# Kernel tuning notes

Hardware: AMD Instinct MI355X
Metric: run time of the kernel (lower is better)

## Reference

```python
import jax, jax.numpy as jnp
import numpy as np

N_HEAD, D_MODEL, D_HEAD = 16, 1024, 64
BSZ, SEQLEN = 2, 2048
ROPE_BASE = 10000.0


def _rope_tables(seqlen, d_head, base=ROPE_BASE):
    # freqs_cis = exp(i * t * theta_j), theta_j = base^(-2j/d_head)
    inv_freq = 1.0 / (base ** (np.arange(0, d_head, 2, dtype=np.float32) / d_head))
    t = np.arange(seqlen, dtype=np.float32)
    ang = np.outer(t, inv_freq)  # [S, d_head//2]
    return jnp.asarray(np.cos(ang)), jnp.asarray(np.sin(ang))


def setup_inputs() -> dict:
    key = jax.random.key(0)
    ks = jax.random.split(key, 5)
    x = jax.random.normal(ks[0], (BSZ, SEQLEN, D_MODEL), dtype=jnp.float32)
    freqs_cos, freqs_sin = _rope_tables(SEQLEN, D_HEAD)
    scale = 0.02
    # weights stored as (in, out) so projection is x @ w
    wq = jax.random.normal(ks[1], (D_MODEL, N_HEAD * D_HEAD), dtype=jnp.float32) * scale
    wk = jax.random.normal(ks[2], (D_MODEL, N_HEAD * D_HEAD), dtype=jnp.float32) * scale
    wv = jax.random.normal(ks[3], (D_MODEL, N_HEAD * D_HEAD), dtype=jnp.float32) * scale
    wo = jax.random.normal(ks[4], (N_HEAD * D_HEAD, D_MODEL), dtype=jnp.float32) * scale
    return {"x": x, "freqs_cos": freqs_cos, "freqs_sin": freqs_sin,
            "wq": wq, "wk": wk, "wv": wv, "wo": wo}


def _apply_rope(t, cos, sin):
    # t: [B, S, H, Dh]; complex pairs are consecutive elements (x0 + i*x1)
    B, S, H, Dh = t.shape
    tf = t.astype(jnp.float32).reshape(B, S, H, Dh // 2, 2)
    t0, t1 = tf[..., 0], tf[..., 1]
    c = cos[None, :, None, :]  # [1, S, 1, Dh//2]
    s = sin[None, :, None, :]
    o0 = t0 * c - t1 * s
    o1 = t0 * s + t1 * c
    return jnp.stack([o0, o1], axis=-1).reshape(B, S, H, Dh).astype(t.dtype)


def reference(x, freqs_cos, freqs_sin, wq, wk, wv, wo):
    B, S, _ = x.shape
    H, Dh = N_HEAD, D_HEAD
    q = jnp.einsum('bsd,de->bse', x, wq).reshape(B, S, H, Dh)
    k = jnp.einsum('bsd,de->bse', x, wk).reshape(B, S, H, Dh)
    v = jnp.einsum('bsd,de->bse', x, wv).reshape(B, S, H, Dh)
    q = _apply_rope(q, freqs_cos, freqs_sin)
    k = _apply_rope(k, freqs_cos, freqs_sin)
    # [B, H, S, Dh]
    q = q.transpose(0, 2, 1, 3)
    k = k.transpose(0, 2, 1, 3)
    v = v.transpose(0, 2, 1, 3)
    scores = jnp.einsum('bhqd,bhkd->bhqk', q, k) / jnp.sqrt(jnp.float32(Dh))
    probs = jax.nn.softmax(scores.astype(jnp.float32), axis=-1).astype(q.dtype)
    out = jnp.einsum('bhqk,bhkd->bhqd', probs, v)  # [B, H, S, Dh]
    out = out.transpose(0, 2, 1, 3).reshape(B, S, H * Dh)
    return jnp.einsum('bse,ed->bsd', out, wo)
```

## Files before the change

kernel.cpp:

```cpp
#include <hip/hip_runtime.h>
#include <math.h>

#define BSZ 2
#define SEQ 2048
#define NH 16
#define DH 64
#define DM 1024
#define HD 1024

typedef _Float16 h16;
typedef _Float16 half8 __attribute__((ext_vector_type(8)));
typedef _Float16 half4 __attribute__((ext_vector_type(4)));
typedef float f32x4 __attribute__((ext_vector_type(4)));
typedef unsigned int u32;
typedef unsigned int u32x2v __attribute__((ext_vector_type(2)));
typedef unsigned int u32x4v __attribute__((ext_vector_type(4)));

__device__ __forceinline__ f32x4 mfma16(half8 a, half8 b, f32x4 c) {
    return __builtin_amdgcn_mfma_f32_16x16x32_f16(a, b, c, 0, 0, 0);
}

__device__ __forceinline__ void async_copy16(h16* lds, const h16* g) {
    __builtin_amdgcn_global_load_lds(
        (const __attribute__((address_space(1))) unsigned int*)g,
        (__attribute__((address_space(3))) unsigned int*)lds, 16, 0, 0);
}

#define SWZ(cb, r) ((((cb) ^ ((r) & 7)) * 8))

#define QSWZ(cb, r) ((((cb) ^ ((r) & 3) ^ (((r) >> 2) & 3)) * 8))

#define OBA(r, c) ((r) * 64 + ((((c) >> 2) ^ ((r) & 15)) << 2))

#define EXP2(x) __builtin_amdgcn_exp2f(x)

__device__ __forceinline__ u32 pack2(float a, float b) {
    auto p = __builtin_amdgcn_cvt_pkrtz(a, b);
    return __builtin_bit_cast(u32, p);
}

__device__ __forceinline__ void pl32swap(u32& a, u32& b) {
#if __has_builtin(__builtin_amdgcn_permlane32_swap)
    u32x2v r = __builtin_amdgcn_permlane32_swap(a, b, false, false);
    a = r.x; b = r.y;
#else
    u32 sa = __builtin_amdgcn_ds_swizzle(a, 0x801F);
    u32 sb = __builtin_amdgcn_ds_swizzle(b, 0x801F);
    bool hi = (threadIdx.x & 32) != 0;
    u32 na = hi ? sb : a;
    u32 nb = hi ? b : sa;
    a = na; b = nb;
#endif
}

__device__ __forceinline__ void pl16swap(u32& a, u32& b) {
#if __has_builtin(__builtin_amdgcn_permlane16_swap)
    u32x2v r = __builtin_amdgcn_permlane16_swap(a, b, false, false);
    a = r.x; b = r.y;
#else
    u32 sa = __builtin_amdgcn_ds_swizzle(a, 0x401F);
    u32 sb = __builtin_amdgcn_ds_swizzle(b, 0x401F);
    bool hi = (threadIdx.x & 16) != 0;
    u32 na = hi ? sb : a;
    u32 nb = hi ? b : sa;
    a = na; b = nb;
#endif
}

__global__ __launch_bounds__(256) void prep_kernel(
    const float* __restrict__ x, const float* __restrict__ wq,
    const float* __restrict__ wk, const float* __restrict__ wv,
    const float* __restrict__ wo,
    h16* __restrict__ x16, h16* __restrict__ wt)
{
    const int z = blockIdx.z;
    const int t = threadIdx.x;
    if (z == 4) {
        int flat = blockIdx.y * 16 + blockIdx.x;
#pragma unroll
        for (int i = 0; i < 8; ++i) {
            int idx = flat * 16384 + i * 2048 + t * 8;
            float4 a = *(const float4*)&x[idx];
            float4 b = *(const float4*)&x[idx + 4];
            half8 o;
            o[0] = (h16)a.x; o[1] = (h16)a.y; o[2] = (h16)a.z; o[3] = (h16)a.w;
            o[4] = (h16)b.x; o[5] = (h16)b.y; o[6] = (h16)b.z; o[7] = (h16)b.w;
            *(half8*)&x16[idx] = o;
        }
        return;
    }
    const float* w = (z == 0) ? wq : (z == 1) ? wk : (z == 2) ? wv : wo;
    h16* ot = wt + (size_t)z * DM * DM;
    __shared__ float tile[64][68];
    const int k0 = blockIdx.y * 64, n0 = blockIdx.x * 64;
    const int r = t >> 2, c4 = (t & 3) * 16;
#pragma unroll
    for (int i = 0; i < 16; i += 4) {
        float4 v = *(const float4*)&w[(size_t)(k0 + r) * DM + n0 + c4 + i];
        tile[r][c4 + i + 0] = v.x; tile[r][c4 + i + 1] = v.y;
        tile[r][c4 + i + 2] = v.z; tile[r][c4 + i + 3] = v.w;
    }
    __syncthreads();
#pragma unroll
    for (int g = 0; g < 2; ++g) {
        half8 hh;
#pragma unroll
        for (int j = 0; j < 8; ++j)
            hh[j] = (h16)tile[c4 + g * 8 + j][r];
        *(half8*)&ot[(size_t)(n0 + r) * DM + k0 + c4 + g * 8] = hh;
    }
}

__global__ __launch_bounds__(512, 4) void qkv_kernel(
    const h16* __restrict__ x16, const h16* __restrict__ wt,
    const float* __restrict__ fcos, const float* __restrict__ fsin,
    h16* __restrict__ Q16, h16* __restrict__ K16, h16* __restrict__ VT16)
{
    const int id  = (blockIdx.z * 32 + blockIdx.y) * 8 + blockIdx.x;
    const int swz = (id & 7) * 96 + (id >> 3);
    const int z   = swz >> 8;
    const int m0  = ((swz >> 3) & 31) * 128;
    const int n0  = (swz & 7) * 128;

    const h16* __restrict__ bw = wt + (size_t)z * DM * DM;

    __shared__ h16 smem[17408];
    h16* Vt = smem;

    const int t  = threadIdx.x;
    const int w  = t >> 6, ln = t & 63;
    const int L  = ln & 15, U = ln >> 4;
    const int wm = (w & 3) * 32;
    const int wn = (w >> 2) * 64;

    const int lr   = ln >> 2;
    const int cs   = ln & 3;
    const int gch  = cs ^ (lr & 3) ^ ((lr >> 2) & 3);
    const int srow = w * 16 + lr;

    f32x4 acc[2][4];
#pragma unroll
    for (int i = 0; i < 2; ++i)
#pragma unroll
        for (int j = 0; j < 4; ++j) acc[i][j] = (f32x4)0.0f;

    async_copy16(&smem[w * 512],        &x16[(size_t)(m0 + srow) * DM + gch * 8]);
    async_copy16(&smem[4096 + w * 512], &bw [(size_t)(n0 + srow) * DM + gch * 8]);

    for (int k0 = 0; k0 < DM; k0 += 32) {
        const int buf = (k0 >> 5) & 1;
        h16* As = smem + buf * 8192;
        h16* Bs = As + 4096;

        __builtin_amdgcn_sched_barrier(0);
        asm volatile("s_waitcnt vmcnt(0)" ::: "memory");
        __builtin_amdgcn_s_barrier();
        __builtin_amdgcn_sched_barrier(0);

        if (k0 + 32 < DM) {
            h16* An = smem + (buf ^ 1) * 8192;
            async_copy16(&An[w * 512],
                         &x16[(size_t)(m0 + srow) * DM + k0 + 32 + gch * 8]);
            async_copy16(&An[4096 + w * 512],
                         &bw [(size_t)(n0 + srow) * DM + k0 + 32 + gch * 8]);
        }

        __builtin_amdgcn_s_setprio(1);
        half8 af[2], bf[4];
#pragma unroll
        for (int mt = 0; mt < 2; ++mt)
            af[mt] = *(const half8*)&As[(wm + mt * 16 + L) * 32 + QSWZ(U, L)];
#pragma unroll
        for (int nt = 0; nt < 4; ++nt)
            bf[nt] = *(const half8*)&Bs[(wn + nt * 16 + L) * 32 + QSWZ(U, L)];
#pragma unroll
        for (int mt = 0; mt < 2; ++mt)
#pragma unroll
            for (int nt = 0; nt < 4; ++nt)
                acc[mt][nt] = mfma16(bf[nt], af[mt], acc[mt][nt]);
        __builtin_amdgcn_s_setprio(0);
    }

    const int b = m0 >> 11;
    const int sbase = m0 & 2047;

    if (z < 2) {
        const float sc = (z == 0) ? 0.125f * 1.44269504088896f : 1.0f;
#pragma unroll
        for (int mt = 0; mt < 2; ++mt) {
            int s = sbase + wm + mt * 16 + L;
            const float* ct = &fcos[s * 32];
            const float* st = &fsin[s * 32];
#pragma unroll
            for (int nt = 0; nt < 4; ++nt) {
                int nl = n0 + wn + nt * 16 + U * 4;
                int d = nl & 63, h = nl >> 6;
                int pd = d >> 1;
                float cv0 = ct[pd], sv0 = st[pd];
                float cv1 = ct[pd + 1], sv1 = st[pd + 1];
                float v0 = acc[mt][nt][0], v1 = acc[mt][nt][1];
                float v2 = acc[mt][nt][2], v3 = acc[mt][nt][3];
                float o0 = (v0 * cv0 - v1 * sv0) * sc;
                float o1 = (v0 * sv0 + v1 * cv0) * sc;
                float o2 = (v2 * cv1 - v3 * sv1) * sc;
                float o3 = (v2 * sv1 + v3 * cv1) * sc;
                size_t addr = ((size_t)(b * NH + h) * SEQ + s) * DH + d;
                half4 kk;
                kk[0] = (h16)o0; kk[1] = (h16)o1; kk[2] = (h16)o2; kk[3] = (h16)o3;
                if (z == 0) *(half4*)&Q16[addr] = kk;
                else        *(half4*)&K16[addr] = kk;
            }
        }
    } else {
        __syncthreads();
#pragma unroll
        for (int mt = 0; mt < 2; ++mt)
#pragma unroll
            for (int nt = 0; nt < 4; ++nt)
#pragma unroll
                for (int r = 0; r < 4; ++r) {
                    int nloc = wn + nt * 16 + U * 4 + r;
                    int sloc = wm + mt * 16 + L;
                    Vt[nloc * 136 + sloc] = (h16)acc[mt][nt][r];
                }
        __syncthreads();
#pragma unroll
        for (int i = 0; i < 4; ++i) {
            int c = i * 512 + t;
            int dl = c >> 4;
            int s8 = (c & 15) * 8;
            half8 vv = *(const half8*)&Vt[dl * 136 + s8];
            int n = n0 + dl;
            int d = n & 63, h = n >> 6;
            *(half8*)&VT16[((size_t)(b * NH + h) * DH + d) * SEQ + sbase + s8] = vv;
        }
    }
}

__global__ __launch_bounds__(512, 4) void attn_kernel(
    const h16* __restrict__ Q16, const h16* __restrict__ K16,
    const h16* __restrict__ VT16, h16* __restrict__ A16)
{
    __shared__ h16 smem[32768];
    float* lbuf = (float*)(smem + 16384);
    float* Obuf = (float*)smem;

    const int t = threadIdx.x, w = t >> 6, ln = t & 63;
    const int L = ln & 15, U = ln >> 4;
    const int pair = w >> 1, half = w & 1;
    const int qw = pair * 32, kh = half * 64;

    const int id  = blockIdx.y * 16 + blockIdx.x;
    const int swz = (id & 7) * 64 + (id >> 3);
    const int q0  = (swz & 15) * 128;
    const int bh  = swz >> 4;
    const size_t base = (size_t)bh * SEQ * DH;

    half8 qf[2][2];
#pragma unroll
    for (int qb = 0; qb < 2; ++qb)
#pragma unroll
        for (int ks = 0; ks < 2; ++ks)
            qf[qb][ks] = *(const half8*)&Q16[base + (size_t)(q0 + qw + qb * 16 + L) * DH + ks * 32 + U * 8];

    half8 one8;
#pragma unroll
    for (int i = 0; i < 8; ++i) one8[i] = (h16)1.0f;

    f32x4 O[4][2];
    f32x4 lsum[2];
#pragma unroll
    for (int dt = 0; dt < 4; ++dt)
#pragma unroll
        for (int qb = 0; qb < 2; ++qb) O[dt][qb] = (f32x4)0.0f;
    lsum[0] = (f32x4)0.0f;
    lsum[1] = (f32x4)0.0f;

    const int sr  = ln >> 3;
    const int scb = (ln & 7) ^ sr;

#pragma unroll
    for (int c = 0; c < 2; ++c) {
        int rbk = c * 64 + w * 8;
        async_copy16(&smem[rbk * 64], &K16[base + (size_t)(rbk + sr) * DH + scb * 8]);
    }
#pragma unroll
    for (int c = 0; c < 2; ++c) {
        int rv = (w * 2 + c) * 4;
        int c16 = (ln & 15) ^ ((rv + U) & 15);
        async_copy16(&smem[16384 + rv * 128], &VT16[base + (size_t)(rv + U) * SEQ + c16 * 8]);
    }

    for (int j0 = 0; j0 < SEQ; j0 += 128) {
        const int buf = (j0 >> 7) & 1;
        h16* Kcur  = smem + buf * 8192;
        h16* VTcur = smem + 16384 + buf * 8192;

        __builtin_amdgcn_sched_barrier(0);
        asm volatile("s_waitcnt vmcnt(0)" ::: "memory");
        __builtin_amdgcn_s_barrier();
        __builtin_amdgcn_sched_barrier(0);

        if (j0 + 128 < SEQ) {
            h16* Knxt  = smem + (buf ^ 1) * 8192;
            h16* Vnxt  = smem + 16384 + (buf ^ 1) * 8192;
#pragma unroll
            for (int c = 0; c < 2; ++c) {
                int rbk = c * 64 + w * 8;
                async_copy16(&Knxt[rbk * 64],
                             &K16[base + (size_t)(j0 + 128 + rbk + sr) * DH + scb * 8]);
            }
#pragma unroll
            for (int c = 0; c < 2; ++c) {
                int rv = (w * 2 + c) * 4;
                int c16 = (ln & 15) ^ ((rv + U) & 15);
                async_copy16(&Vnxt[rv * 128],
                             &VT16[base + (size_t)(rv + U) * SEQ + (j0 + 128) + c16 * 8]);
            }
        }

        f32x4 S[4][2];
        __builtin_amdgcn_s_setprio(1);
#pragma unroll
        for (int nt = 0; nt < 4; ++nt) {
            S[nt][0] = (f32x4)0.0f;
            S[nt][1] = (f32x4)0.0f;
#pragma unroll
            for (int ks = 0; ks < 2; ++ks) {
                half8 kf = *(const half8*)&Kcur[(kh + nt * 16 + L) * 64 + SWZ(ks * 4 + U, L)];
                S[nt][0] = mfma16(kf, qf[0][ks], S[nt][0]);
                S[nt][1] = mfma16(kf, qf[1][ks], S[nt][1]);
            }
        }
        __builtin_amdgcn_s_setprio(0);

        half8 pf[2][2];
#pragma unroll
        for (int qb = 0; qb < 2; ++qb) {
            u32 X[2][2][2];
#pragma unroll
            for (int k5 = 0; k5 < 2; ++k5)
#pragma unroll
                for (int p = 0; p < 2; ++p) {
                    u32 a = pack2(EXP2(S[k5 * 2 + 0][qb][2 * p]),
                                  EXP2(S[k5 * 2 + 0][qb][2 * p + 1]));
                    u32 b = pack2(EXP2(S[k5 * 2 + 1][qb][2 * p]),
                                  EXP2(S[k5 * 2 + 1][qb][2 * p + 1]));
                    pl32swap(a, b);
                    X[k5][0][p] = a; X[k5][1][p] = b;
                }
#pragma unroll
            for (int k5 = 0; k5 < 2; ++k5) {
                u32x4v uv;
#pragma unroll
                for (int p = 0; p < 2; ++p) {
                    u32 a = X[k5][0][p], b = X[k5][1][p];
                    pl16swap(a, b);
                    uv[p]     = a;
                    uv[2 + p] = b;
                }
                pf[qb][k5] = __builtin_bit_cast(half8, uv);
            }
        }

        __builtin_amdgcn_s_setprio(1);
#pragma unroll
        for (int dt = 0; dt < 4; ++dt)
#pragma unroll
            for (int ks2 = 0; ks2 < 2; ++ks2) {
                half8 vf = *(const half8*)&VTcur[(dt * 16 + L) * 128 + ((half * 8 + ks2 * 4 + U) ^ L) * 8];
                O[dt][0] = mfma16(vf, pf[0][ks2], O[dt][0]);
                O[dt][1] = mfma16(vf, pf[1][ks2], O[dt][1]);
            }
#pragma unroll
        for (int ks2 = 0; ks2 < 2; ++ks2) {
            lsum[0] = mfma16(one8, pf[0][ks2], lsum[0]);
            lsum[1] = mfma16(one8, pf[1][ks2], lsum[1]);
        }
        __builtin_amdgcn_s_setprio(0);
    }

    if (U == 0) {
        lbuf[w * 32 + L]      = lsum[0][0];
        lbuf[w * 32 + 16 + L] = lsum[1][0];
    }
    __syncthreads();
    const int pw = w ^ 1;
    float l_tot[2];
    l_tot[0] = lsum[0][0] + lbuf[pw * 32 + L];
    l_tot[1] = lsum[1][0] + lbuf[pw * 32 + 16 + L];

    if (half) {
#pragma unroll
        for (int qb = 0; qb < 2; ++qb)
#pragma unroll
            for (int dt = 0; dt < 4; ++dt)
                *(f32x4*)&Obuf[OBA(qw + qb * 16 + L, dt * 16 + U * 4)] = O[dt][qb];
    }
    __syncthreads();
    if (!half) {
        const int b = bh >> 4, hh = bh & 15;
#pragma unroll
        for (int qb = 0; qb < 2; ++qb) {
            float inv = 1.0f / l_tot[qb];
            int s = q0 + qw + qb * 16 + L;
#pragma unroll
            for (int dt = 0; dt < 4; ++dt) {
                f32x4 op = *(const f32x4*)&Obuf[OBA(qw + qb * 16 + L, dt * 16 + U * 4)];
                half4 o4;
#pragma unroll
                for (int r = 0; r < 4; ++r)
                    o4[r] = (h16)((O[dt][qb][r] + op[r]) * inv);
                *(half4*)&A16[(size_t)(b * SEQ + s) * HD + hh * DH + dt * 16 + U * 4] = o4;
            }
        }
    }
}

__global__ __launch_bounds__(512, 4) void oproj_kernel(
    const h16* __restrict__ A16, const h16* __restrict__ bw,
    float* __restrict__ out)
{
    __shared__ h16 smem[24576];

    const int id  = blockIdx.y * 16 + blockIdx.x;
    const int swz = (id & 7) * 64 + (id >> 3);
    const int n0  = (swz & 15) * 64;
    const int m0  = (swz >> 4) * 128;

    const int t  = threadIdx.x;
    const int w  = t >> 6, ln = t & 63;
    const int L  = ln & 15, U = ln >> 4;

    const int sr  = ln >> 3;
    const int scb = (ln & 7) ^ sr;

    f32x4 acc[4];
#pragma unroll
    for (int j = 0; j < 4; ++j) acc[j] = (f32x4)0.0f;

#pragma unroll
    for (int c = 0; c < 2; ++c) {
        int rb = w * 16 + c * 8;
        async_copy16(&smem[rb * 64], &A16[(size_t)(m0 + rb + sr) * DM + scb * 8]);
    }
    async_copy16(&smem[8192 + (w * 8) * 64], &bw[(size_t)(n0 + w * 8 + sr) * DM + scb * 8]);

    for (int k0 = 0; k0 < DM; k0 += 64) {
        const int buf = (k0 >> 6) & 1;
        h16* As = smem + buf * 12288;
        h16* Bs = As + 8192;

        asm volatile("s_waitcnt vmcnt(0)" ::: "memory");
        __builtin_amdgcn_s_barrier();
        __builtin_amdgcn_sched_barrier(0);

        if (k0 + 64 < DM) {
            h16* An = smem + (buf ^ 1) * 12288;
#pragma unroll
            for (int c = 0; c < 2; ++c) {
                int rb = w * 16 + c * 8;
                async_copy16(&An[rb * 64],
                             &A16[(size_t)(m0 + rb + sr) * DM + k0 + 64 + scb * 8]);
            }
            async_copy16(&An[8192 + (w * 8) * 64],
                         &bw[(size_t)(n0 + w * 8 + sr) * DM + k0 + 64 + scb * 8]);
        }

        __builtin_amdgcn_s_setprio(1);
#pragma unroll
        for (int ks = 0; ks < 2; ++ks) {
            half8 af, bf[4];
            af = *(const half8*)&As[(w * 16 + L) * 64 + SWZ(ks * 4 + U, L)];
#pragma unroll
            for (int nt = 0; nt < 4; ++nt)
                bf[nt] = *(const half8*)&Bs[(nt * 16 + L) * 64 + SWZ(ks * 4 + U, L)];
#pragma unroll
            for (int nt = 0; nt < 4; ++nt)
                acc[nt] = mfma16(af, bf[nt], acc[nt]);
        }
        __builtin_amdgcn_s_setprio(0);
    }

#pragma unroll
    for (int nt = 0; nt < 4; ++nt)
#pragma unroll
        for (int r = 0; r < 4; ++r) {
            int row = m0 + w * 16 + U * 4 + r;
            int col = n0 + nt * 16 + L;
            out[(size_t)row * DM + col] = acc[nt][r];
        }
}

extern "C" void kernel_launch(void* const* d_in, const int* in_sizes, int n_in,
                              void* d_out, int out_size, void* d_ws, size_t ws_size,
                              hipStream_t stream)
{
    const float* x    = (const float*)d_in[0];
    const float* fcos = (const float*)d_in[1];
    const float* fsin = (const float*)d_in[2];
    const float* wq   = (const float*)d_in[3];
    const float* wk   = (const float*)d_in[4];
    const float* wv   = (const float*)d_in[5];
    const float* wo   = (const float*)d_in[6];
    float* out = (float*)d_out;

    const size_t M4 = (size_t)4 * 1024 * 1024;
    h16* x16  = (h16*)d_ws;
    h16* wt   = x16 + M4;
    h16* Q16  = wt + M4;
    h16* K16  = Q16 + M4;
    h16* VT16 = K16 + M4;
    h16* A16  = VT16 + M4;

    prep_kernel<<<dim3(16, 16, 5), 256, 0, stream>>>(x, wq, wk, wv, wo, x16, wt);
    qkv_kernel<<<dim3(8, 32, 3), 512, 0, stream>>>(x16, wt, fcos, fsin,
                                                   Q16, K16, VT16);
    attn_kernel<<<dim3(16, 32), 512, 0, stream>>>(Q16, K16, VT16, A16);
    oproj_kernel<<<dim3(16, 32), 512, 0, stream>>>(A16, wt + 3 * (size_t)DM * DM, out);
}
```

Baseline: 186.9 us.

## Triple-buffer async LDS loads in QKV and output projection GEMMs

Switches the QKV and O-projection GEMM main loops from double to triple buffering. Two tiles are issued ahead, and a partial vmcnt wait lets one tile stay in flight while the current one is computed. This is meant to hide more global-load latency behind the MFMA work. In exchange it uses more LDS per block (48KB and 72KB), which may reduce how many blocks fit on a CU; the qkv launch bound is raised to 6 to ask for more occupancy.

After: 185.0 us. About the same (-1.0%).

```diff
diff --git a/kernel.cpp b/kernel.cpp
--- a/kernel.cpp
+++ b/kernel.cpp
@@ -111,7 +111,7 @@
     }
 }
 
-__global__ __launch_bounds__(512, 4) void qkv_kernel(
+__global__ __launch_bounds__(512, 6) void qkv_kernel(
     const h16* __restrict__ x16, const h16* __restrict__ wt,
     const float* __restrict__ fcos, const float* __restrict__ fsin,
     h16* __restrict__ Q16, h16* __restrict__ K16, h16* __restrict__ VT16)
@@ -124,7 +124,7 @@
 
     const h16* __restrict__ bw = wt + (size_t)z * DM * DM;
 
-    __shared__ h16 smem[17408];
+    __shared__ h16 smem[24576];
     h16* Vt = smem;
 
     const int t  = threadIdx.x;
@@ -144,25 +144,30 @@
 #pragma unroll
         for (int j = 0; j < 4; ++j) acc[i][j] = (f32x4)0.0f;
 
-    async_copy16(&smem[w * 512],        &x16[(size_t)(m0 + srow) * DM + gch * 8]);
-    async_copy16(&smem[4096 + w * 512], &bw [(size_t)(n0 + srow) * DM + gch * 8]);
-
-    for (int k0 = 0; k0 < DM; k0 += 32) {
-        const int buf = (k0 >> 5) & 1;
+    auto stage = [&](int buf, int kk) {
+        h16* dst = smem + buf * 8192;
+        async_copy16(&dst[w * 512],        &x16[(size_t)(m0 + srow) * DM + kk + gch * 8]);
+        async_copy16(&dst[4096 + w * 512], &bw [(size_t)(n0 + srow) * DM + kk + gch * 8]);
+    };
+
+    stage(0, 0);
+    stage(1, 32);
+
+    int step = 0;
+    for (int k0 = 0; k0 < DM; k0 += 32, ++step) {
+        const int buf = step - (step / 3) * 3;
         h16* As = smem + buf * 8192;
         h16* Bs = As + 4096;
 
         __builtin_amdgcn_sched_barrier(0);
-        asm volatile("s_waitcnt vmcnt(0)" ::: "memory");
+        if (k0 + 32 < DM) asm volatile("s_waitcnt vmcnt(2)" ::: "memory");
+        else              asm volatile("s_waitcnt vmcnt(0)" ::: "memory");
         __builtin_amdgcn_s_barrier();
         __builtin_amdgcn_sched_barrier(0);
 
-        if (k0 + 32 < DM) {
-            h16* An = smem + (buf ^ 1) * 8192;
-            async_copy16(&An[w * 512],
-                         &x16[(size_t)(m0 + srow) * DM + k0 + 32 + gch * 8]);
-            async_copy16(&An[4096 + w * 512],
-                         &bw [(size_t)(n0 + srow) * DM + k0 + 32 + gch * 8]);
+        if (k0 + 64 < DM) {
+            int nb = step + 2;
+            stage(nb - (nb / 3) * 3, k0 + 64);
         }
 
         __builtin_amdgcn_s_setprio(1);
@@ -421,7 +426,7 @@
     const h16* __restrict__ A16, const h16* __restrict__ bw,
     float* __restrict__ out)
 {
-    __shared__ h16 smem[24576];
+    __shared__ h16 smem[36864];
 
     const int id  = blockIdx.y * 16 + blockIdx.x;
     const int swz = (id & 7) * 64 + (id >> 3);
@@ -439,32 +444,34 @@
 #pragma unroll
     for (int j = 0; j < 4; ++j) acc[j] = (f32x4)0.0f;
 
-#pragma unroll
-    for (int c = 0; c < 2; ++c) {
-        int rb = w * 16 + c * 8;
-        async_copy16(&smem[rb * 64], &A16[(size_t)(m0 + rb + sr) * DM + scb * 8]);
-    }
-    async_copy16(&smem[8192 + (w * 8) * 64], &bw[(size_t)(n0 + w * 8 + sr) * DM + scb * 8]);
-
-    for (int k0 = 0; k0 < DM; k0 += 64) {
-        const int buf = (k0 >> 6) & 1;
+    auto stage = [&](int buf, int kk) {
+        h16* dst = smem + buf * 12288;
+#pragma unroll
+        for (int c = 0; c < 2; ++c) {
+            int rb = w * 16 + c * 8;
+            async_copy16(&dst[rb * 64], &A16[(size_t)(m0 + rb + sr) * DM + kk + scb * 8]);
+        }
+        async_copy16(&dst[8192 + (w * 8) * 64], &bw[(size_t)(n0 + w * 8 + sr) * DM + kk + scb * 8]);
+    };
+
+    stage(0, 0);
+    stage(1, 64);
+
+    int step = 0;
+    for (int k0 = 0; k0 < DM; k0 += 64, ++step) {
+        const int buf = step - (step / 3) * 3;
         h16* As = smem + buf * 12288;
         h16* Bs = As + 8192;
 
-        asm volatile("s_waitcnt vmcnt(0)" ::: "memory");
+        __builtin_amdgcn_sched_barrier(0);
+        if (k0 + 64 < DM) asm volatile("s_waitcnt vmcnt(3)" ::: "memory");
+        else              asm volatile("s_waitcnt vmcnt(0)" ::: "memory");
         __builtin_amdgcn_s_barrier();
         __builtin_amdgcn_sched_barrier(0);
 
-        if (k0 + 64 < DM) {
-            h16* An = smem + (buf ^ 1) * 12288;
-#pragma unroll
-            for (int c = 0; c < 2; ++c) {
-                int rb = w * 16 + c * 8;
-                async_copy16(&An[rb * 64],
-                             &A16[(size_t)(m0 + rb + sr) * DM + k0 + 64 + scb * 8]);
-            }
-            async_copy16(&An[8192 + (w * 8) * 64],
-                         &bw[(size_t)(n0 + w * 8 + sr) * DM + k0 + 64 + scb * 8]);
+        if (k0 + 128 < DM) {
+            int nb = step + 2;
+            stage(nb - (nb / 3) * 3, k0 + 128);
         }
 
         __builtin_amdgcn_s_setprio(1);
```
